# Performance work log

Measured on AMD Instinct MI355X. Metric: run time of the kernel, lower is better.

Reference implementation:

```python
import jax, jax.numpy as jnp
import numpy as np

N = 100000      # nodes
E = 1600000     # edges (before self loops)
F_IN = 128      # num_features
HEADS1, CH1 = 8, 8    # conv1: heads=8, out=8, concat -> 64
HEADS2, CH2 = 1, 16   # conv2: heads=1, out=16, concat=False
B = 64          # graphs in batch


def setup_inputs() -> dict:
    key = jax.random.key(0)
    ks = jax.random.split(key, 20)
    s = 0.05
    x = jax.random.normal(ks[0], (N, F_IN), dtype=jnp.float32)
    edge_index = jax.random.randint(ks[1], (2, E), 0, N, dtype=jnp.int64)
    batch = jnp.sort(jax.random.randint(ks[2], (N,), 0, B, dtype=jnp.int64))
    d = {
        'x': x, 'edge_index': edge_index, 'batch': batch,
        # conv1 params (GATv2: lin_l / lin_r with bias, att vector, output bias)
        'Wl1': jax.random.normal(ks[3], (F_IN, HEADS1 * CH1)) * s,
        'bl1': jnp.zeros((HEADS1 * CH1,), jnp.float32),
        'Wr1': jax.random.normal(ks[4], (F_IN, HEADS1 * CH1)) * s,
        'br1': jnp.zeros((HEADS1 * CH1,), jnp.float32),
        'att1': jax.random.normal(ks[5], (HEADS1, CH1)) * s,
        'bias1': jnp.zeros((HEADS1 * CH1,), jnp.float32),
        # conv2 params
        'Wl2': jax.random.normal(ks[6], (HEADS1 * CH1, HEADS2 * CH2)) * s,
        'bl2': jnp.zeros((HEADS2 * CH2,), jnp.float32),
        'Wr2': jax.random.normal(ks[7], (HEADS1 * CH1, HEADS2 * CH2)) * s,
        'br2': jnp.zeros((HEADS2 * CH2,), jnp.float32),
        'att2': jax.random.normal(ks[8], (HEADS2, CH2)) * s,
        'bias2': jnp.zeros((CH2,), jnp.float32),
        # classifier 16 -> 1
        'Wc': jax.random.normal(ks[9], (CH2, 1)) * s,
        'bc': jnp.zeros((1,), jnp.float32),
    }
    return d


def gatv2_layer(x, src, dst, Wl, bl, Wr, br, att, bias, heads, ch, concat):
    n = x.shape[0]
    xl = (x @ Wl + bl).reshape(n, heads, ch)   # source transform (messages)
    xr = (x @ Wr + br).reshape(n, heads, ch)   # target transform
    m = xl[src] + xr[dst]                      # [E, H, C]
    e = jax.nn.leaky_relu(m, 0.2)
    logits = jnp.einsum('ehc,hc->eh', e, att)  # [E, H]
    # segment softmax over incoming edges per target node
    mx = jax.ops.segment_max(logits, dst, num_segments=n)
    mx = jnp.where(jnp.isfinite(mx), mx, 0.0)
    ex = jnp.exp(logits - mx[dst])
    denom = jax.ops.segment_sum(ex, dst, num_segments=n)
    alpha = ex / (denom[dst] + 1e-16)
    out = jax.ops.segment_sum(alpha[:, :, None] * xl[src], dst, num_segments=n)
    out = out.reshape(n, heads * ch) if concat else out.mean(axis=1)
    return out + bias


def reference(x, edge_index, batch, Wl1, bl1, Wr1, br1, att1, bias1,
              Wl2, bl2, Wr2, br2, att2, bias2, Wc, bc):
    n = x.shape[0]
    loops = jnp.arange(n, dtype=edge_index.dtype)
    src = jnp.concatenate([edge_index[0], loops])   # add self loops (PyG default)
    dst = jnp.concatenate([edge_index[1], loops])

    h = gatv2_layer(x, src, dst, Wl1, bl1, Wr1, br1, att1, bias1, HEADS1, CH1, True)
    h = jax.nn.elu(h)
    h = gatv2_layer(h, src, dst, Wl2, bl2, Wr2, br2, att2, bias2, HEADS2, CH2, False)

    counts = jax.ops.segment_sum(jnp.ones((n,), h.dtype), batch, num_segments=B)
    pooled = jax.ops.segment_sum(h, batch, num_segments=B) / jnp.clip(counts, 1.0)[:, None]
    out = (pooled @ Wc + bc).reshape(-1)            # [B]
    return out, pooled
```

## Files before the change

kernel.cpp:

```cpp
#include <hip/hip_runtime.h>
#include <cstdint>
#include <cstddef>

#define F_IN   128
#define HC1    64
#define CH2_   16
#define NB     64
#define BUKPAD 8192

typedef __attribute__((ext_vector_type(8))) short bf16x8;
typedef __attribute__((ext_vector_type(4))) float f32x4;

__global__ void fill_f32(float* __restrict__ p, float v, int n) {
  int i = blockIdx.x * blockDim.x + threadIdx.x;
  int stride = gridDim.x * blockDim.x;
  for (; i < n; i += stride) p[i] = v;
}

__device__ __forceinline__ unsigned short f2bf_rne(float v) {
  unsigned int u = __float_as_uint(v);
  unsigned int r = (u + 0x7FFFu + ((u >> 16) & 1u)) >> 16;
  return (unsigned short)r;
}
__device__ __forceinline__ float bf2f(unsigned short b) {
  return __uint_as_float((unsigned int)b << 16);
}

template<int CTRL>
__device__ __forceinline__ float dpp_add(float v) {
  int j = __builtin_amdgcn_update_dpp(0, __float_as_int(v), CTRL, 0xF, 0xF, true);
  return v + __int_as_float(j);
}
__device__ __forceinline__ float sum16_dpp(float v) {
  v = dpp_add<0xB1>(v);
  v = dpp_add<0x4E>(v);
  v = dpp_add<0x141>(v);
  v = dpp_add<0x140>(v);
  return v;
}

__global__ void build_wfrag(const float* __restrict__ Wl, const float* __restrict__ Wr,
                            unsigned short* __restrict__ wfrag) {
  int idx = blockIdx.x * 256 + threadIdx.x;
  if (idx >= 16384) return;
  int e    = idx & 7;
  int lane = (idx >> 3) & 63;
  int tile = (idx >> 9) & 7;
  int ks   = idx >> 12;
  int k    = ks * 32 + (lane >> 4) * 8 + e;
  int col  = tile * 16 + (lane & 15);
  float v = (col < 64) ? Wl[k * 64 + col] : Wr[k * 64 + (col - 64)];
  wfrag[idx] = f2bf_rne(v);
}

__global__ __launch_bounds__(256) void gemm_mfma_l1(
    const float* __restrict__ x, const unsigned short* __restrict__ wfrag,
    const float* __restrict__ bl, const float* __restrict__ br,
    unsigned short* __restrict__ ya, float* __restrict__ yb, int n) {
  constexpr int RP = 136;
  __shared__ __align__(16) char smem[34816 + 32768];
  unsigned short* axhi = (unsigned short*)smem;
  unsigned short* axlo = (unsigned short*)(smem + 17408);
  unsigned short* wf   = (unsigned short*)(smem + 34816);
  float* outs = (float*)smem;

  const int t = threadIdx.x;
  const int node0 = blockIdx.x * 64;

  for (int i = t; i < 2048; i += 256)
    reinterpret_cast<int4*>(wf)[i] = reinterpret_cast<const int4*>(wfrag)[i];
  for (int i = t; i < 64 * 32; i += 256) {
    int row = i >> 5, kk = (i & 31) * 4;
    int node = node0 + row;
    float4 v = make_float4(0.f, 0.f, 0.f, 0.f);
    if (node < n) v = *reinterpret_cast<const float4*>(x + (size_t)node * 128 + kk);
    ushort4 hi, lo;
    hi.x = f2bf_rne(v.x); lo.x = f2bf_rne(v.x - bf2f(hi.x));
    hi.y = f2bf_rne(v.y); lo.y = f2bf_rne(v.y - bf2f(hi.y));
    hi.z = f2bf_rne(v.z); lo.z = f2bf_rne(v.z - bf2f(hi.z));
    hi.w = f2bf_rne(v.w); lo.w = f2bf_rne(v.w - bf2f(hi.w));
    *reinterpret_cast<ushort4*>(axhi + row * RP + kk) = hi;
    *reinterpret_cast<ushort4*>(axlo + row * RP + kk) = lo;
  }
  __syncthreads();

  const int wv   = t >> 6;
  const int lane = t & 63;
  const int mrow = lane & 15;
  const int kg   = lane >> 4;
  f32x4 acc[8];
#pragma unroll
  for (int i = 0; i < 8; ++i) acc[i] = (f32x4){0.f, 0.f, 0.f, 0.f};
  const int abase = (wv * 16 + mrow) * RP;
#pragma unroll
  for (int ks = 0; ks < 4; ++ks) {
    int aoff = abase + ks * 32 + kg * 8;
    bf16x8 ahi = *reinterpret_cast<const bf16x8*>(axhi + aoff);
    bf16x8 alo = *reinterpret_cast<const bf16x8*>(axlo + aoff);
#pragma unroll
    for (int tl = 0; tl < 8; ++tl) {
      bf16x8 b = *reinterpret_cast<const bf16x8*>(wf + ((ks * 8 + tl) * 64 + lane) * 8);
      acc[tl] = __builtin_amdgcn_mfma_f32_16x16x32_bf16(alo, b, acc[tl], 0, 0, 0);
      acc[tl] = __builtin_amdgcn_mfma_f32_16x16x32_bf16(ahi, b, acc[tl], 0, 0, 0);
    }
  }
  __syncthreads();
#pragma unroll
  for (int tl = 0; tl < 8; ++tl)
#pragma unroll
    for (int r = 0; r < 4; ++r) {
      int row = wv * 16 + kg * 4 + r;
      outs[row * 128 + tl * 16 + mrow] = acc[tl][r];
    }
  __syncthreads();
  for (int i = t; i < 64 * 64; i += 256) {
    int row = i >> 6, col = i & 63;
    int node = node0 + row;
    if (node < n) ya[(size_t)node * 64 + col] = f2bf_rne(outs[row * 128 + col] + bl[col]);
  }
  for (int i = t; i < 64 * 64; i += 256) {
    int row = i >> 6, col = i & 63;
    int node = node0 + row;
    if (node < n) yb[(size_t)node * 64 + col] = outs[row * 128 + 64 + col] + br[col];
  }
}


__global__ void bucket_scatter(const int* __restrict__ ei, int E, int E2,
                               int* __restrict__ gcnt, int* __restrict__ gbuk) {
  __shared__ int hbase[512];
  __shared__ int hcnt[512];
  const int t = threadIdx.x;
  for (int i = t; i < 512; i += 256) { hbase[i] = 0; hcnt[i] = 0; }
  __syncthreads();
  int srcs[32], dsts[32];
  const int tile0 = blockIdx.x * 8192;
#pragma unroll
  for (int k = 0; k < 32; ++k) {
    int e = tile0 + k * 256 + t;
    int s = -1, d = 0;
    if (e < E2) {
      if (e < E) { s = ei[e]; d = ei[E + e]; } else { s = d = e - E; }
      atomicAdd(&hbase[d >> 8], 1);
    }
    srcs[k] = s; dsts[k] = d;
  }
  __syncthreads();
  for (int i = t; i < 512; i += 256) {
    int c = hbase[i];
    hbase[i] = (c > 0) ? atomicAdd(&gcnt[i], c) : 0;
  }
  __syncthreads();
#pragma unroll
  for (int k = 0; k < 32; ++k) {
    if (srcs[k] >= 0) {
      int d = dsts[k], b = d >> 8;
      int r = atomicAdd(&hcnt[b], 1);
      int pl = hbase[b] + r;
      if (pl < BUKPAD) gbuk[(size_t)b * BUKPAD + pl] = (srcs[k] << 8) | (d & 255);
    }
  }
}

__global__ void bucket_prefix(const int* __restrict__ gcnt, int nbuk,
                              int* __restrict__ gbase, int* __restrict__ row_start, int n) {
  int lane = threadIdx.x;
  int carry = 0;
  for (int basei = 0; basei < nbuk; basei += 64) {
    int i = basei + lane;
    int orig = (i < nbuk) ? gcnt[i] : 0;
    int v = orig;
    for (int off = 1; off < 64; off <<= 1) {
      int u = __shfl_up(v, off);
      if (lane >= off) v += u;
    }
    if (i < nbuk) gbase[i] = carry + v - orig;
    carry += __shfl(v, 63);
  }
  if (lane == 0) row_start[n] = carry;
}

__global__ void bucket_csr(const int* __restrict__ gcnt, const int* __restrict__ gbase,
                           const int* __restrict__ gbuk,
                           int* __restrict__ row_start, int* __restrict__ csr_src, int n) {
  const int b = blockIdx.x;
  const int t = threadIdx.x;
  const int node0 = b << 8;
  const int cntb = min(gcnt[b], BUKPAD);
  const int base = gbase[b];
  const int* buk = gbuk + (size_t)b * BUKPAD;
  __shared__ int h[256];
  __shared__ int off[256];
  h[t] = 0;
  __syncthreads();
  for (int i = t; i < cntb; i += 256) atomicAdd(&h[buk[i] & 255], 1);
  __syncthreads();
  off[t] = h[t];
  __syncthreads();
  for (int o = 1; o < 256; o <<= 1) {
    int u = (t >= o) ? off[t - o] : 0;
    __syncthreads();
    off[t] += u;
    __syncthreads();
  }
  int excl = off[t] - h[t];
  if (node0 + t < n) row_start[node0 + t] = base + excl;
  h[t] = excl;
  __syncthreads();
  for (int i = t; i < cntb; i += 256) {
    int p = buk[i];
    int r = atomicAdd(&h[p & 255], 1);
    csr_src[base + r] = p >> 8;
  }
}

__global__ void fused_layer1(const int* __restrict__ row_start, const int* __restrict__ csr_src,
                             const unsigned short* __restrict__ xl, const float* __restrict__ xr,
                             const float* __restrict__ att, const float* __restrict__ bias,
                             const float* __restrict__ Wl2, const float* __restrict__ bl2,
                             const float* __restrict__ Wr2, const float* __restrict__ br2,
                             float* __restrict__ xl2, float* __restrict__ xr2, int n) {
  __shared__ float Ws2[64 * 32];
  __shared__ float b2s[32];
  const int t = threadIdx.x;
  for (int i = t; i < 64 * 16; i += 256) {
    int l = i >> 4, j = i & 15;
    Ws2[l * 32 + j]      = Wl2[i];
    Ws2[l * 32 + 16 + j] = Wr2[i];
  }
  if (t < 16) { b2s[t] = bl2[t]; b2s[16 + t] = br2[t]; }
  __syncthreads();

  const int node = blockIdx.x * 4 + (t >> 6);
  if (node >= n) return;
  const int lane = t & 63;
  const int g = lane >> 4;
  const int q = lane & 15;
  const float4 attv = *reinterpret_cast<const float4*>(att + q * 4);
  const float4 xrv  = *reinterpret_cast<const float4*>(xr + (size_t)node * 64 + q * 4);
  const unsigned short* xlq = xl + q * 4;
  const int beg = row_start[node];
  const int total = row_start[node + 1] - beg;
  const float NEGB = -3.0e38f;
  float den = 0.0f;
  float4 acc = make_float4(0.f, 0.f, 0.f, 0.f);

  for (int base = 0; base < total; base += 64) {
    int idx = base + lane;
    int sidx = csr_src[beg + (idx < total ? idx : total - 1)];
    const int lim = min(64, total - base);
    for (int c0 = 0; c0 < lim; c0 += 16) {
      int ii[4]; int sv[4]; ushort4 u[4];
#pragma unroll
      for (int j = 0; j < 4; ++j) ii[j] = c0 + j * 4 + g;
#pragma unroll
      for (int j = 0; j < 4; ++j) sv[j] = __shfl(sidx, ii[j]);
#pragma unroll
      for (int j = 0; j < 4; ++j)
        u[j] = *reinterpret_cast<const ushort4*>(xlq + (size_t)sv[j] * 64);
#pragma unroll
      for (int j = 0; j < 4; ++j) {
        float x0 = bf2f(u[j].x), x1 = bf2f(u[j].y), x2 = bf2f(u[j].z), x3 = bf2f(u[j].w);
        float a0 = x0 + xrv.x; a0 = fmaxf(a0, 0.2f * a0);
        float a1 = x1 + xrv.y; a1 = fmaxf(a1, 0.2f * a1);
        float a2 = x2 + xrv.z; a2 = fmaxf(a2, 0.2f * a2);
        float a3 = x3 + xrv.w; a3 = fmaxf(a3, 0.2f * a3);
        float p = a0 * attv.x + a1 * attv.y + a2 * attv.z + a3 * attv.w;
        float v = dpp_add<0xB1>(p);
        float ex = __expf(ii[j] < lim ? v : NEGB);
        den  += ex;
        acc.x += ex * x0; acc.y += ex * x1;
        acc.z += ex * x2; acc.w += ex * x3;
      }
    }
  }
  acc.x += __shfl_xor(acc.x, 16); acc.y += __shfl_xor(acc.y, 16);
  acc.z += __shfl_xor(acc.z, 16); acc.w += __shfl_xor(acc.w, 16);
  acc.x += __shfl_xor(acc.x, 32); acc.y += __shfl_xor(acc.y, 32);
  acc.z += __shfl_xor(acc.z, 32); acc.w += __shfl_xor(acc.w, 32);
  den += __shfl_xor(den, 16);
  den += __shfl_xor(den, 32);
  const float inv = 1.0f / (den + 1e-16f);
  const float4 bi = *reinterpret_cast<const float4*>(bias + q * 4);
  float o0 = acc.x * inv + bi.x; o0 = o0 > 0.f ? o0 : __expf(o0) - 1.0f;
  float o1 = acc.y * inv + bi.y; o1 = o1 > 0.f ? o1 : __expf(o1) - 1.0f;
  float o2 = acc.z * inv + bi.z; o2 = o2 > 0.f ? o2 : __expf(o2) - 1.0f;
  float o3 = acc.w * inv + bi.w; o3 = o3 > 0.f ? o3 : __expf(o3) - 1.0f;

  int srcl = lane >> 2;
  float c0v = __shfl(o0, srcl);
  float c1v = __shfl(o1, srcl);
  float c2v = __shfl(o2, srcl);
  float c3v = __shfl(o3, srcl);
  int r = lane & 3;
  float o = (r == 0) ? c0v : (r == 1) ? c1v : (r == 2) ? c2v : c3v;

  const int j    = lane & 31;
  const int half = lane >> 5;
  float part2 = 0.0f;
#pragma unroll 8
  for (int l = 0; l < 32; ++l) {
    int src = half * 32 + l;
    float ov = __shfl(o, src);
    part2 += ov * Ws2[src * 32 + j];
  }
  part2 += __shfl_xor(part2, 32);
  if (lane < 16)      xl2[(size_t)node * 16 + j]        = part2 + b2s[j];
  else if (lane < 32) xr2[(size_t)node * 16 + (j - 16)] = part2 + b2s[j];
}

__global__ void fused_layer2(const int* __restrict__ row_start, const int* __restrict__ csr_src,
                             const float* __restrict__ xl, const float* __restrict__ xr,
                             const float* __restrict__ att, const float* __restrict__ bias,
                             float* __restrict__ out, int n) {
  int node = blockIdx.x * 16 + (threadIdx.x >> 4);
  if (node >= n) return;
  const int lane = threadIdx.x & 63;
  const int c = lane & 15;
  const int gbase = lane & 48;
  const float attv = att[c];
  const float xrv  = xr[(size_t)node * 16 + c];
  const int beg = row_start[node];
  const int total = row_start[node + 1] - beg;
  const float NEGB = -3.0e38f;
  float den = 0.0f, acc = 0.0f;

  for (int base = 0; base < total; base += 16) {
    int wi = base + c;
    int sidx = csr_src[beg + (wi < total ? wi : total - 1)];
    const int lim = min(16, total - base);
    for (int c0 = 0; c0 < lim; c0 += 4) {
      int sv[4]; float xv[4];
#pragma unroll
      for (int j = 0; j < 4; ++j) sv[j] = __shfl(sidx, gbase + c0 + j);
#pragma unroll
      for (int j = 0; j < 4; ++j)
        xv[j] = xl[(size_t)sv[j] * 16 + c];
#pragma unroll
      for (int j = 0; j < 4; ++j) {
        float a = xv[j] + xrv; a = fmaxf(a, 0.2f * a);
        float v = sum16_dpp(a * attv);
        float ex = __expf((c0 + j) < lim ? v : NEGB);
        den += ex;
        acc += ex * xv[j];
      }
    }
  }
  out[(size_t)node * 16 + c] = acc / (den + 1e-16f) + bias[c];
}


__global__ void pool_kernel(const float* __restrict__ h2, const int* __restrict__ batch,
                            float* __restrict__ sums, float* __restrict__ cnts, int n) {
  __shared__ float ls[NB * CH2_];
  __shared__ float lc[NB];
  for (int i = threadIdx.x; i < NB * CH2_; i += blockDim.x) ls[i] = 0.0f;
  for (int i = threadIdx.x; i < NB; i += blockDim.x) lc[i] = 0.0f;
  __syncthreads();
  int total = n * 16;
  int stride = gridDim.x * blockDim.x;
  for (int i = blockIdx.x * blockDim.x + threadIdx.x; i < total; i += stride) {
    int node = i >> 4, c = i & 15;
    int b = batch[node];
    atomicAdd(&ls[b * 16 + c], h2[i]);
    if (c == 0) atomicAdd(&lc[b], 1.0f);
  }
  __syncthreads();
  for (int i = threadIdx.x; i < NB * CH2_; i += blockDim.x)
    if (ls[i] != 0.0f) atomicAdd(&sums[i], ls[i]);
  for (int i = threadIdx.x; i < NB; i += blockDim.x)
    if (lc[i] != 0.0f) atomicAdd(&cnts[i], lc[i]);
}

__global__ void classifier(const float* __restrict__ sums, const float* __restrict__ cnts,
                           const float* __restrict__ Wc, const float* __restrict__ bc,
                           float* __restrict__ out) {
  int b = threadIdx.x;
  if (b >= NB) return;
  float cnt = cnts[b];
  cnt = cnt > 1.0f ? cnt : 1.0f;
  float acc = 0.0f;
  for (int c = 0; c < 16; ++c) {
    float p = sums[b * 16 + c] / cnt;
    out[NB + b * 16 + c] = p;
    acc += p * Wc[c];
  }
  out[b] = acc + bc[0];
}

extern "C" void kernel_launch(void* const* d_in, const int* in_sizes, int n_in,
                              void* d_out, int out_size, void* d_ws, size_t ws_size,
                              hipStream_t stream) {
  const float* x     = (const float*)d_in[0];
  const int*   ei    = (const int*)d_in[1];
  const int*   batch = (const int*)d_in[2];
  const float* Wl1   = (const float*)d_in[3];
  const float* bl1   = (const float*)d_in[4];
  const float* Wr1   = (const float*)d_in[5];
  const float* br1   = (const float*)d_in[6];
  const float* att1  = (const float*)d_in[7];
  const float* bias1 = (const float*)d_in[8];
  const float* Wl2   = (const float*)d_in[9];
  const float* bl2   = (const float*)d_in[10];
  const float* Wr2   = (const float*)d_in[11];
  const float* br2   = (const float*)d_in[12];
  const float* att2  = (const float*)d_in[13];
  const float* bias2 = (const float*)d_in[14];
  const float* Wc    = (const float*)d_in[15];
  const float* bc    = (const float*)d_in[16];
  float* out = (float*)d_out;

  const int N  = in_sizes[0] / F_IN;
  const int E  = in_sizes[1] / 2;
  const int E2 = E + N;
  const int nbuk = (N + 255) >> 8;

  float* ws   = (float*)d_ws;
  unsigned short* xl1 = (unsigned short*)ws;
  float* xr1  = (float*)(xl1 + (size_t)N * 64);
  float* xl2  = xr1 + (size_t)N * 64;
  float* xr2  = xl2 + (size_t)N * 16;
  float* h2   = xr2 + (size_t)N * 16;
  int* irow   = (int*)(h2 + (size_t)N * 16);
  int* icsr   = irow + (N + 1);
  int* gcnt   = icsr + E2;
  int* gbase  = gcnt + 512;
  int* gbuk   = gbase + 513 + 2;
  unsigned short* wfrag =
      (unsigned short*)(((uintptr_t)(gbuk + (size_t)nbuk * BUKPAD) + 15) & ~(uintptr_t)15);
  float* sums = (float*)(wfrag + 16384);
  float* cnts = sums + NB * CH2_;

  fill_f32<<<1, 256, 0, stream>>>((float*)gcnt, 0.0f, 512);
  bucket_scatter<<<(E2 + 8191) / 8192, 256, 0, stream>>>(ei, E, E2, gcnt, gbuk);
  bucket_prefix<<<1, 64, 0, stream>>>(gcnt, nbuk, gbase, irow, N);
  bucket_csr<<<nbuk, 256, 0, stream>>>(gcnt, gbase, gbuk, irow, icsr, N);

  build_wfrag<<<64, 256, 0, stream>>>(Wl1, Wr1, wfrag);
  gemm_mfma_l1<<<(N + 63) / 64, 256, 0, stream>>>(x, wfrag, bl1, br1, xl1, xr1, N);

  fused_layer1<<<(N + 3) / 4, 256, 0, stream>>>(
      irow, icsr, xl1, xr1, att1, bias1, Wl2, bl2, Wr2, br2, xl2, xr2, N);

  fused_layer2<<<(N + 15) / 16, 256, 0, stream>>>(irow, icsr, xl2, xr2, att2, bias2, h2, N);

  fill_f32<<<1, 256, 0, stream>>>(sums, 0.0f, NB * CH2_ + NB);
  pool_kernel<<<256, 256, 0, stream>>>(h2, batch, sums, cnts, N);
  classifier<<<1, 64, 0, stream>>>(sums, cnts, Wc, bc, out);
}
```

Measured before the change: 226.6 us.

## Merge edge bucket scatter with layer-1 GEMM into one launch; store xl2 as bf16

The edge bucket-scatter blocks and the layer-1 MFMA GEMM blocks are combined into a single kernel, with the block index choosing the role, so the two independent stages can run concurrently and one launch is removed. The scatter blocks now allocate the GEMM's larger shared-memory footprint, which may lower their occupancy. Separately, the layer-2 source features xl2 are stored as bf16 instead of fp32, halving the bytes of the random gathers in fused_layer2 at some cost in precision.

New measurement: 213.7 us, median of 2. -5.7%, faster.

```diff
diff --git a/kernel.cpp b/kernel.cpp
--- a/kernel.cpp
+++ b/kernel.cpp
@@ -53,19 +53,56 @@
   wfrag[idx] = f2bf_rne(v);
 }
 
-__global__ __launch_bounds__(256) void gemm_mfma_l1(
-    const float* __restrict__ x, const unsigned short* __restrict__ wfrag,
-    const float* __restrict__ bl, const float* __restrict__ br,
-    unsigned short* __restrict__ ya, float* __restrict__ yb, int n) {
+
+__device__ void scatter_body(char* smem, const int* __restrict__ ei, int E, int E2,
+                             int* __restrict__ gcnt, int* __restrict__ gbuk, int blk) {
+  int* hbase = (int*)smem;
+  int* hcnt  = hbase + 512;
+  const int t = threadIdx.x;
+  for (int i = t; i < 512; i += 256) { hbase[i] = 0; hcnt[i] = 0; }
+  __syncthreads();
+  int srcs[32], dsts[32];
+  const int tile0 = blk * 8192;
+#pragma unroll
+  for (int k = 0; k < 32; ++k) {
+    int e = tile0 + k * 256 + t;
+    int s = -1, d = 0;
+    if (e < E2) {
+      if (e < E) { s = ei[e]; d = ei[E + e]; } else { s = d = e - E; }
+      atomicAdd(&hbase[d >> 8], 1);
+    }
+    srcs[k] = s; dsts[k] = d;
+  }
+  __syncthreads();
+  for (int i = t; i < 512; i += 256) {
+    int c = hbase[i];
+    hbase[i] = (c > 0) ? atomicAdd(&gcnt[i], c) : 0;
+  }
+  __syncthreads();
+#pragma unroll
+  for (int k = 0; k < 32; ++k) {
+    if (srcs[k] >= 0) {
+      int d = dsts[k], b = d >> 8;
+      int r = atomicAdd(&hcnt[b], 1);
+      int pl = hbase[b] + r;
+      if (pl < BUKPAD) gbuk[(size_t)b * BUKPAD + pl] = (srcs[k] << 8) | (d & 255);
+    }
+  }
+}
+
+__device__ void gemm_body(char* smem, const float* __restrict__ x,
+                          const unsigned short* __restrict__ wfrag,
+                          const float* __restrict__ bl, const float* __restrict__ br,
+                          unsigned short* __restrict__ ya, float* __restrict__ yb,
+                          int n, int blk) {
   constexpr int RP = 136;
-  __shared__ __align__(16) char smem[34816 + 32768];
   unsigned short* axhi = (unsigned short*)smem;
   unsigned short* axlo = (unsigned short*)(smem + 17408);
   unsigned short* wf   = (unsigned short*)(smem + 34816);
   float* outs = (float*)smem;
 
   const int t = threadIdx.x;
-  const int node0 = blockIdx.x * 64;
+  const int node0 = blk * 64;
 
   for (int i = t; i < 2048; i += 256)
     reinterpret_cast<int4*>(wf)[i] = reinterpret_cast<const int4*>(wfrag)[i];
@@ -125,42 +162,19 @@
   }
 }
 
-
-__global__ void bucket_scatter(const int* __restrict__ ei, int E, int E2,
-                               int* __restrict__ gcnt, int* __restrict__ gbuk) {
-  __shared__ int hbase[512];
-  __shared__ int hcnt[512];
-  const int t = threadIdx.x;
-  for (int i = t; i < 512; i += 256) { hbase[i] = 0; hcnt[i] = 0; }
-  __syncthreads();
-  int srcs[32], dsts[32];
-  const int tile0 = blockIdx.x * 8192;
-#pragma unroll
-  for (int k = 0; k < 32; ++k) {
-    int e = tile0 + k * 256 + t;
-    int s = -1, d = 0;
-    if (e < E2) {
-      if (e < E) { s = ei[e]; d = ei[E + e]; } else { s = d = e - E; }
-      atomicAdd(&hbase[d >> 8], 1);
-    }
-    srcs[k] = s; dsts[k] = d;
-  }
-  __syncthreads();
-  for (int i = t; i < 512; i += 256) {
-    int c = hbase[i];
-    hbase[i] = (c > 0) ? atomicAdd(&gcnt[i], c) : 0;
-  }
-  __syncthreads();
-#pragma unroll
-  for (int k = 0; k < 32; ++k) {
-    if (srcs[k] >= 0) {
-      int d = dsts[k], b = d >> 8;
-      int r = atomicAdd(&hcnt[b], 1);
-      int pl = hbase[b] + r;
-      if (pl < BUKPAD) gbuk[(size_t)b * BUKPAD + pl] = (srcs[k] << 8) | (d & 255);
-    }
-  }
-}
+__global__ __launch_bounds__(256) void mega_scatter_gemm(
+    const int* __restrict__ ei, int E, int E2,
+    int* __restrict__ gcnt, int* __restrict__ gbuk, int nscat,
+    const float* __restrict__ x, const unsigned short* __restrict__ wfrag,
+    const float* __restrict__ bl, const float* __restrict__ br,
+    unsigned short* __restrict__ ya, float* __restrict__ yb, int n) {
+  __shared__ __align__(16) char smem[34816 + 32768];
+  if ((int)blockIdx.x < nscat)
+    scatter_body(smem, ei, E, E2, gcnt, gbuk, blockIdx.x);
+  else
+    gemm_body(smem, x, wfrag, bl, br, ya, yb, n, blockIdx.x - nscat);
+}
+
 
 __global__ void bucket_prefix(const int* __restrict__ gcnt, int nbuk,
                               int* __restrict__ gbase, int* __restrict__ row_start, int n) {
@@ -219,7 +233,7 @@
                              const float* __restrict__ att, const float* __restrict__ bias,
                              const float* __restrict__ Wl2, const float* __restrict__ bl2,
                              const float* __restrict__ Wr2, const float* __restrict__ br2,
-                             float* __restrict__ xl2, float* __restrict__ xr2, int n) {
+                             unsigned short* __restrict__ xl2, float* __restrict__ xr2, int n) {
   __shared__ float Ws2[64 * 32];
   __shared__ float b2s[32];
   const int t = threadIdx.x;
@@ -305,12 +319,12 @@
     part2 += ov * Ws2[src * 32 + j];
   }
   part2 += __shfl_xor(part2, 32);
-  if (lane < 16)      xl2[(size_t)node * 16 + j]        = part2 + b2s[j];
+  if (lane < 16)      xl2[(size_t)node * 16 + j]        = f2bf_rne(part2 + b2s[j]);
   else if (lane < 32) xr2[(size_t)node * 16 + (j - 16)] = part2 + b2s[j];
 }
 
 __global__ void fused_layer2(const int* __restrict__ row_start, const int* __restrict__ csr_src,
-                             const float* __restrict__ xl, const float* __restrict__ xr,
+                             const unsigned short* __restrict__ xl, const float* __restrict__ xr,
                              const float* __restrict__ att, const float* __restrict__ bias,
                              float* __restrict__ out, int n) {
   int node = blockIdx.x * 16 + (threadIdx.x >> 4);
@@ -335,7 +349,7 @@
       for (int j = 0; j < 4; ++j) sv[j] = __shfl(sidx, gbase + c0 + j);
 #pragma unroll
       for (int j = 0; j < 4; ++j)
-        xv[j] = xl[(size_t)sv[j] * 16 + c];
+        xv[j] = bf2f(xl[(size_t)sv[j] * 16 + c]);
 #pragma unroll
       for (int j = 0; j < 4; ++j) {
         float a = xv[j] + xrv; a = fmaxf(a, 0.2f * a);
@@ -414,12 +428,14 @@
   const int E  = in_sizes[1] / 2;
   const int E2 = E + N;
   const int nbuk = (N + 255) >> 8;
+  const int nscat = (E2 + 8191) / 8192;
+  const int ngemm = (N + 63) / 64;
 
   float* ws   = (float*)d_ws;
   unsigned short* xl1 = (unsigned short*)ws;
   float* xr1  = (float*)(xl1 + (size_t)N * 64);
-  float* xl2  = xr1 + (size_t)N * 64;
-  float* xr2  = xl2 + (size_t)N * 16;
+  unsigned short* xl2 = (unsigned short*)(xr1 + (size_t)N * 64);
+  float* xr2  = (float*)(xl2 + (size_t)N * 16);
   float* h2   = xr2 + (size_t)N * 16;
   int* irow   = (int*)(h2 + (size_t)N * 16);
   int* icsr   = irow + (N + 1);
@@ -432,12 +448,13 @@
   float* cnts = sums + NB * CH2_;
 
   fill_f32<<<1, 256, 0, stream>>>((float*)gcnt, 0.0f, 512);
-  bucket_scatter<<<(E2 + 8191) / 8192, 256, 0, stream>>>(ei, E, E2, gcnt, gbuk);
+  build_wfrag<<<64, 256, 0, stream>>>(Wl1, Wr1, wfrag);
+
+  mega_scatter_gemm<<<nscat + ngemm, 256, 0, stream>>>(
+      ei, E, E2, gcnt, gbuk, nscat, x, wfrag, bl1, br1, xl1, xr1, N);
+
   bucket_prefix<<<1, 64, 0, stream>>>(gcnt, nbuk, gbase, irow, N);
   bucket_csr<<<nbuk, 256, 0, stream>>>(gcnt, gbase, gbuk, irow, icsr, N);
-
-  build_wfrag<<<64, 256, 0, stream>>>(Wl1, Wr1, wfrag);
-  gemm_mfma_l1<<<(N + 63) / 64, 256, 0, stream>>>(x, wfrag, bl1, br1, xl1, xr1, N);
 
   fused_layer1<<<(N + 3) / 4, 256, 0, stream>>>(
       irow, icsr, xl1, xr1, att1, bias1, Wl2, bl2, Wr2, br2, xl2, xr2, N);
```
